# Kernel tuning notes

Hardware: AMD Instinct MI355X
Metric: run time of the kernel (lower is better)

## Reference

```python
import jax, jax.numpy as jnp
import numpy as np

N_NODES = 50000
IN_FEAT = 64
HIDDEN = 128
OUT = 10
N_EDGES = 800000


def setup_inputs() -> dict:
    key = jax.random.key(0)
    ks = jax.random.split(key, 8)
    s = lambda fan_in: 1.0 / np.sqrt(fan_in)
    x = jax.random.normal(ks[0], (N_NODES, IN_FEAT), dtype=jnp.float32)
    edge_index = jax.random.randint(ks[1], (2, N_EDGES), 0, N_NODES, dtype=jnp.int32)
    # SAGEConv params: lin_l (neighbor path, has bias) and lin_r (root path, no bias)
    W1l = jax.random.uniform(ks[2], (HIDDEN, IN_FEAT), jnp.float32, -s(IN_FEAT), s(IN_FEAT))
    b1 = jnp.zeros((HIDDEN,), jnp.float32)
    W1r = jax.random.uniform(ks[3], (HIDDEN, IN_FEAT), jnp.float32, -s(IN_FEAT), s(IN_FEAT))
    W2l = jax.random.uniform(ks[4], (OUT, HIDDEN), jnp.float32, -s(HIDDEN), s(HIDDEN))
    b2 = jnp.zeros((OUT,), jnp.float32)
    W2r = jax.random.uniform(ks[5], (OUT, HIDDEN), jnp.float32, -s(HIDDEN), s(HIDDEN))
    return {"x": x, "edge_index": edge_index, "W1l": W1l, "b1": b1, "W1r": W1r,
            "W2l": W2l, "b2": b2, "W2r": W2r}


def _sage_conv(x, src, dst, Wl, b, Wr, num_nodes):
    # mean-aggregate neighbor features (src -> dst), then linear + root linear
    msgs = x[src]                                                    # [E, d]
    agg = jax.ops.segment_sum(msgs, dst, num_segments=num_nodes)     # [N, d]
    cnt = jax.ops.segment_sum(jnp.ones((src.shape[0],), x.dtype), dst,
                              num_segments=num_nodes)                 # [N]
    mean = agg / jnp.maximum(cnt, 1.0)[:, None]
    return mean @ Wl.T + b + x @ Wr.T


def reference(x, edge_index, W1l, b1, W1r, W2l, b2, W2r):
    src, dst = edge_index[0], edge_index[1]
    n = x.shape[0]
    h = jax.nn.relu(_sage_conv(x, src, dst, W1l, b1, W1r, n))   # [N, hidden]
    h = _sage_conv(h, src, dst, W2l, b2, W2r, n)                 # [N, 10]
    # sum over nodes (transpose(0,1) then sum dim=1 == sum over axis 0)
    return jnp.sum(h, axis=0).reshape(1, OUT)
```

## Files before the change

### kernel.cpp

```cpp
#include <hip/hip_runtime.h>
#include <hip/hip_fp8.h>


constexpr int N = 50000;
constexpr int F = 64;
constexpr int H = 128;
constexpr int O = 10;
constexpr int E = 800000;

constexpr int NBUK = 391;
constexpr int CAPC = 2528;
constexpr int ADEPTH = 16;
constexpr int GSTR = 4;
constexpr int SPLIT = 4;

constexpr int NTILE = (N + 63) / 64;
constexpr int NB_TRANS = 391;

constexpr int GBIN_LEN  = NBUK * CAPC;
constexpr int GCUR_LEN  = NBUK * GSTR;
constexpr int MEANH_LEN = N * F / 2;
constexpr int XQ_LEN    = N * F / 4;
constexpr size_t WS_NEED_Q =
    (size_t)GBIN_LEN * 2 + GCUR_LEN * 2 + 2 * H + N + N + MEANH_LEN + XQ_LEN;

typedef _Float16 half2v __attribute__((ext_vector_type(2)));

__device__ __forceinline__ unsigned short f32_to_bf16_rne(float f) {
  unsigned u = __float_as_uint(f);
  u += 0x7FFFu + ((u >> 16) & 1u);
  return (unsigned short)(u >> 16);
}

__device__ __forceinline__ unsigned pack2h(float a, float b) {
  half2v h;
  h.x = (_Float16)a;
  h.y = (_Float16)b;
  return __builtin_bit_cast(unsigned, h);
}

__device__ __forceinline__ float dot2h(unsigned a, unsigned b, float c) {
#if __has_builtin(__builtin_amdgcn_fdot2)
  return __builtin_amdgcn_fdot2(__builtin_bit_cast(half2v, a),
                                __builtin_bit_cast(half2v, b), c, false);
#else
  const half2v ha = __builtin_bit_cast(half2v, a);
  const half2v hb = __builtin_bit_cast(half2v, b);
  c = fmaf((float)ha.x, (float)hb.x, c);
  return fmaf((float)ha.y, (float)hb.y, c);
#endif
}

__global__ __launch_bounds__(256) void k_cast(
    const float* __restrict__ x, unsigned* __restrict__ xq4) {
  const int tid = blockIdx.x * blockDim.x + threadIdx.x;
  const int stride = gridDim.x * blockDim.x;
  for (int i = tid; i < N * F / 4; i += stride) {
    const float4 v = reinterpret_cast<const float4*>(x)[i];
    const __hip_fp8_e4m3 a(v.x), b(v.y), c(v.z), d(v.w);
    const unsigned o = (unsigned)a.__x | ((unsigned)b.__x << 8) |
                       ((unsigned)c.__x << 16) | ((unsigned)d.__x << 24);
    __builtin_nontemporal_store(o, xq4 + i);
  }
}

__global__ __launch_bounds__(256) void k_coarse(
    const int* __restrict__ ei, int* __restrict__ gcur,
    unsigned* __restrict__ gbin, int* __restrict__ gcur2,
    unsigned* __restrict__ gbin2) {
  __shared__ int scnt[NBUK];
  __shared__ unsigned stage[NBUK * ADEPTH];
  __shared__ int scnt2[NBUK];
  __shared__ unsigned stage2[NBUK * ADEPTH];
  const int tid = threadIdx.x;
  const int lane = tid & 63;
  const int wv = tid >> 6;
  for (int i = tid; i < NBUK; i += 256) { scnt[i] = 0; scnt2[i] = 0; }
  __syncthreads();

  const int chunk = E / 256;
  const int base = blockIdx.x * chunk;
  const int end = base + chunk;
  for (int e = base + tid; e < end; e += 256) {
    const int s = ei[e];
    const int d = ei[E + e];
    {
      const int b = d >> 7;
      const unsigned p = ((unsigned)s << 7) | (unsigned)(d & 127);
      const int pos = atomicAdd(&scnt[b], 1);
      if (pos < ADEPTH) {
        stage[b * ADEPTH + pos] = p;
      } else {
        const int g = atomicAdd(&gcur[b * GSTR], 1);
        if (g < CAPC) gbin[(size_t)b * CAPC + g] = p;
      }
    }
    {
      const int b2 = s >> 7;
      const unsigned p2 = ((unsigned)d << 7) | (unsigned)(s & 127);
      const int pos2 = atomicAdd(&scnt2[b2], 1);
      if (pos2 < ADEPTH) {
        stage2[b2 * ADEPTH + pos2] = p2;
      } else {
        const int g2 = atomicAdd(&gcur2[b2 * GSTR], 1);
        if (g2 < CAPC) gbin2[(size_t)b2 * CAPC + g2] = p2;
      }
    }
  }
  __syncthreads();

  for (int b0 = wv * 64 + lane; b0 < NBUK; b0 += 256) {
    int cnt = scnt[b0];
    if (cnt > ADEPTH) cnt = ADEPTH;
    if (cnt > 0) {
      const int gbase = atomicAdd(&gcur[b0 * GSTR], cnt);
      for (int k = 0; k < cnt; ++k) {
        const int g = gbase + k;
        if (g < CAPC) gbin[(size_t)b0 * CAPC + g] = stage[b0 * ADEPTH + k];
      }
    }
    int cnt2 = scnt2[b0];
    if (cnt2 > ADEPTH) cnt2 = ADEPTH;
    if (cnt2 > 0) {
      const int gbase2 = atomicAdd(&gcur2[b0 * GSTR], cnt2);
      for (int k = 0; k < cnt2; ++k) {
        const int g2 = gbase2 + k;
        if (g2 < CAPC) gbin2[(size_t)b0 * CAPC + g2] = stage2[b0 * ADEPTH + k];
      }
    }
  }
}

template <bool USE_Q>
__global__ __launch_bounds__(512) void k_agg2(
    const float* __restrict__ x, const unsigned char* __restrict__ xq,
    const int* __restrict__ gcur, const unsigned* __restrict__ gbin,
    unsigned short* __restrict__ mean1h, float* __restrict__ winv_g) {
  __shared__ int fcnt[32];
  __shared__ float winv_s[32];
  __shared__ unsigned short fbin[32][64];
  const int tid = threadIdx.x;
  const int lane = tid & 63;
  const int wv = __builtin_amdgcn_readfirstlane((int)(tid >> 6));
  const int b = blockIdx.x >> 2;
  const int part = blockIdx.x & 3;
  int mb = gcur[b * GSTR];
  if (mb > CAPC) mb = CAPC;

  if (tid < 32) fcnt[tid] = 0;
  __syncthreads();

  const unsigned* __restrict__ gb = gbin + (size_t)b * CAPC;
#define READF(I)                                                      \
  {                                                                   \
    unsigned P = 0;                                                   \
    const bool v = tid + (I) * 512 < mb;                              \
    if (v) P = gb[tid + (I) * 512];                                   \
    const int row = (int)(P & 127u);                                  \
    if (v && ((row >> 5) == part)) {                                  \
      const int dl = row & 31;                                        \
      const int pos = atomicAdd(&fcnt[dl], 1);                        \
      if (pos < 46) fbin[dl][pos] = (unsigned short)(P >> 7);         \
    }                                                                 \
  }
  READF(0) READF(1) READF(2) READF(3) READF(4)
#undef READF
  __syncthreads();

  if (tid < 32) {
    const int c = fcnt[tid];
    const float wv_ = 1.0f / (float)(c > 0 ? c : 1);
    winv_s[tid] = wv_;
    const int n = b * 128 + part * 32 + tid;
    if (n < N) winv_g[n] = wv_;
  }
  __syncthreads();

  #pragma unroll
  for (int r = 0; r < 4; ++r) {
    const int row = wv * 4 + r;
    const int n = b * 128 + part * 32 + row;
    if (n >= N) break;
    int m = __builtin_amdgcn_readfirstlane(fcnt[row]);
    const float winv = winv_s[row];
    if (m > 46) m = 46;
    const uint4* __restrict__ lq = reinterpret_cast<const uint4*>(&fbin[row][0]);
    const uint4 q0 = lq[0], q1 = lq[1], q2 = lq[2];
    const uint4 q3 = lq[3], q4 = lq[4], q5 = lq[5];
    float acc = 0.f;
#define DO2(U, base)                                                      \
    {                                                                     \
      const unsigned u = __builtin_amdgcn_readfirstlane(U);               \
      int sa = (int)(u & 0xFFFFu), sb = (int)(u >> 16);                   \
      sa = sa < N ? sa : 0;  sb = sb < N ? sb : 0;     \
      float va, vb;                                                       \
      if constexpr (USE_Q) {                                              \
        va = (float)*reinterpret_cast<const __hip_fp8_e4m3*>(             \
                 &xq[(size_t)sa * F + lane]);                             \
        vb = (float)*reinterpret_cast<const __hip_fp8_e4m3*>(             \
                 &xq[(size_t)sb * F + lane]);                             \
      } else {                                                            \
        va = x[(size_t)sa * F + lane];                                    \
        vb = x[(size_t)sb * F + lane];                                    \
      }                                                                   \
      acc += ((base) < m) ? va : 0.f;                                     \
      acc += ((base) + 1 < m) ? vb : 0.f;                                 \
    }
    if (m > 0)  { DO2(q0.x, 0)  DO2(q0.y, 2)  DO2(q0.z, 4)  DO2(q0.w, 6)  }
    if (m > 8)  { DO2(q1.x, 8)  DO2(q1.y, 10) DO2(q1.z, 12) DO2(q1.w, 14) }
    if (m > 16) { DO2(q2.x, 16) DO2(q2.y, 18) DO2(q2.z, 20) DO2(q2.w, 22) }
    if (m > 24) { DO2(q3.x, 24) DO2(q3.y, 26) DO2(q3.z, 28) DO2(q3.w, 30) }
    if (m > 32) { DO2(q4.x, 32) DO2(q4.y, 34) DO2(q4.z, 36) DO2(q4.w, 38) }
    if (m > 40) { DO2(q5.x, 40) DO2(q5.y, 42) DO2(q5.z, 44) }
#undef DO2
    mean1h[(size_t)n * F + lane] = f32_to_bf16_rne(acc * winv);
  }
}

__global__ __launch_bounds__(512) void k_wsum(
    const int* __restrict__ gcur2, const unsigned* __restrict__ gbin2,
    const float* __restrict__ winv_g, float* __restrict__ wsum) {
  __shared__ float lsum[128];
  const int tid = threadIdx.x;
  const int b = blockIdx.x;
  int mb = gcur2[b * GSTR];
  if (mb > CAPC) mb = CAPC;
  if (tid < 128) lsum[tid] = 0.f;
  __syncthreads();
  const unsigned* __restrict__ gb = gbin2 + (size_t)b * CAPC;
  #pragma unroll
  for (int i = 0; i < 5; ++i) {
    const int idx = tid + i * 512;
    if (idx < mb) {
      const unsigned p = gb[idx];
      atomicAdd(&lsum[p & 127u], winv_g[p >> 7]);
    }
  }
  __syncthreads();
  const int n = b * 128 + tid;
  if (tid < 128 && n < N) wsum[n] = lsum[tid];
}

__global__ __launch_bounds__(256) void k_trans(
    const float* __restrict__ x, const unsigned short* __restrict__ mean1h,
    const float* __restrict__ wsum,
    const float* __restrict__ W1l, const float* __restrict__ b1,
    const float* __restrict__ W1r,
    float* __restrict__ S_h, float* __restrict__ S_hw) {
  __shared__ unsigned smem[12288];
  unsigned short* feat_h = reinterpret_cast<unsigned short*>(smem);
  unsigned* wBh = smem + 4096;
  const int tid = threadIdx.x;
  const int tm = tid >> 4;
  const int tj = tid & 15;

  #pragma unroll
  for (int u = 0; u < 8; ++u) {
    const int idx = u * 256 + tid;
    const int jj = idx >> 4;
    const int k4 = idx & 15;
    const float4 vl = *reinterpret_cast<const float4*>(&W1l[jj * F + k4 * 4]);
    const float4 vr = *reinterpret_cast<const float4*>(&W1r[jj * F + k4 * 4]);
    wBh[(k4 * 2 + 0) * 128 + jj] = pack2h(vl.x, vl.y);
    wBh[(k4 * 2 + 1) * 128 + jj] = pack2h(vl.z, vl.w);
    wBh[(32 + k4 * 2 + 0) * 128 + jj] = pack2h(vr.x, vr.y);
    wBh[(32 + k4 * 2 + 1) * 128 + jj] = pack2h(vr.z, vr.w);
  }
  const float4 b1v0 = *reinterpret_cast<const float4*>(&b1[tj * 4]);
  const float4 b1v1 = *reinterpret_cast<const float4*>(&b1[64 + tj * 4]);

  float accS[8] = {0.f, 0.f, 0.f, 0.f, 0.f, 0.f, 0.f, 0.f};
  float accW[8] = {0.f, 0.f, 0.f, 0.f, 0.f, 0.f, 0.f, 0.f};

  for (int t = blockIdx.x; t < NTILE; t += NB_TRANS) {
    const int nbase = t * 64;
    __syncthreads();

    #pragma unroll
    for (int u = 0; u < 8; ++u) {
      const int idx = u * 256 + tid;
      const int nn = idx >> 5;
      const int q = idx & 31;
      const int gn = nbase + nn;
      ushort4 o;
      o.x = 0; o.y = 0; o.z = 0; o.w = 0;
      if (gn < N) {
        float f0, f1, f2, f3;
        if (q < 16) {
          const ushort4 t4 = reinterpret_cast<const ushort4*>(mean1h + (size_t)gn * F)[q];
          f0 = __uint_as_float((unsigned)t4.x << 16);
          f1 = __uint_as_float((unsigned)t4.y << 16);
          f2 = __uint_as_float((unsigned)t4.z << 16);
          f3 = __uint_as_float((unsigned)t4.w << 16);
        } else {
          const float4 v = reinterpret_cast<const float4*>(x + (size_t)gn * F)[q - 16];
          f0 = v.x; f1 = v.y; f2 = v.z; f3 = v.w;
        }
        const unsigned p01 = pack2h(f0, f1);
        const unsigned p23 = pack2h(f2, f3);
        o.x = (unsigned short)(p01 & 0xFFFFu);
        o.y = (unsigned short)(p01 >> 16);
        o.z = (unsigned short)(p23 & 0xFFFFu);
        o.w = (unsigned short)(p23 >> 16);
      }
      const int qs = q ^ ((nn >> 2) & 15);
      *reinterpret_cast<ushort4*>(&feat_h[nn * 128 + qs * 4]) = o;
    }
    __syncthreads();

    float acc[4][8] = {{0.f}};
    #pragma unroll 4
    for (int k4 = 0; k4 < 32; ++k4) {
      uint2 a[4];
      #pragma unroll
      for (int r = 0; r < 4; ++r) {
        const int ks = k4 ^ tm;
        a[r] = *reinterpret_cast<const uint2*>(&feat_h[(tm * 4 + r) * 128 + ks * 4]);
      }
      const uint4 B00 = *reinterpret_cast<const uint4*>(&wBh[(k4 * 2 + 0) * 128 + tj * 4]);
      const uint4 B10 = *reinterpret_cast<const uint4*>(&wBh[(k4 * 2 + 1) * 128 + tj * 4]);
      const uint4 B01 = *reinterpret_cast<const uint4*>(&wBh[(k4 * 2 + 0) * 128 + 64 + tj * 4]);
      const uint4 B11 = *reinterpret_cast<const uint4*>(&wBh[(k4 * 2 + 1) * 128 + 64 + tj * 4]);
      #pragma unroll
      for (int r = 0; r < 4; ++r) {
        acc[r][0] = dot2h(a[r].x, B00.x, acc[r][0]);
        acc[r][0] = dot2h(a[r].y, B10.x, acc[r][0]);
        acc[r][1] = dot2h(a[r].x, B00.y, acc[r][1]);
        acc[r][1] = dot2h(a[r].y, B10.y, acc[r][1]);
        acc[r][2] = dot2h(a[r].x, B00.z, acc[r][2]);
        acc[r][2] = dot2h(a[r].y, B10.z, acc[r][2]);
        acc[r][3] = dot2h(a[r].x, B00.w, acc[r][3]);
        acc[r][3] = dot2h(a[r].y, B10.w, acc[r][3]);
        acc[r][4] = dot2h(a[r].x, B01.x, acc[r][4]);
        acc[r][4] = dot2h(a[r].y, B11.x, acc[r][4]);
        acc[r][5] = dot2h(a[r].x, B01.y, acc[r][5]);
        acc[r][5] = dot2h(a[r].y, B11.y, acc[r][5]);
        acc[r][6] = dot2h(a[r].x, B01.z, acc[r][6]);
        acc[r][6] = dot2h(a[r].y, B11.z, acc[r][6]);
        acc[r][7] = dot2h(a[r].x, B01.w, acc[r][7]);
        acc[r][7] = dot2h(a[r].y, B11.w, acc[r][7]);
      }
    }

    #pragma unroll
    for (int r = 0; r < 4; ++r) {
      const int gn = nbase + tm * 4 + r;
      const bool valid = (gn < N);
      const float wsn = valid ? wsum[gn] : 0.f;
      const float bb[8] = {b1v0.x, b1v0.y, b1v0.z, b1v0.w,
                           b1v1.x, b1v1.y, b1v1.z, b1v1.w};
      #pragma unroll
      for (int c = 0; c < 8; ++c) {
        const float h = valid ? fmaxf(acc[r][c] + bb[c], 0.f) : 0.f;
        accS[c] += h;
        accW[c] = fmaf(wsn, h, accW[c]);
      }
    }
  }

  __syncthreads();
  float* redS = reinterpret_cast<float*>(smem);
  float* redW = reinterpret_cast<float*>(smem) + 2048;
  #pragma unroll
  for (int c = 0; c < 8; ++c) {
    const int j = (c < 4) ? (tj * 4 + c) : (64 + tj * 4 + (c - 4));
    redS[tm * 128 + j] = accS[c];
    redW[tm * 128 + j] = accW[c];
  }
  __syncthreads();
  if (tid < 128) {
    float s = 0.f, w = 0.f;
    #pragma unroll
    for (int m = 0; m < 16; ++m) {
      s += redS[m * 128 + tid];
      w += redW[m * 128 + tid];
    }
    atomicAdd(&S_h[tid], s);
    atomicAdd(&S_hw[tid], w);
  }
}

__global__ __launch_bounds__(64) void k_final(
    const float* __restrict__ S_h, const float* __restrict__ S_hw,
    const float* __restrict__ W2l, const float* __restrict__ b2,
    const float* __restrict__ W2r, float* __restrict__ out) {
  const int j = threadIdx.x;
  if (j < O) {
    float acc = (float)N * b2[j];
    #pragma unroll 8
    for (int k = 0; k < H; ++k)
      acc += S_hw[k] * W2l[j * H + k] + S_h[k] * W2r[j * H + k];
    out[j] = acc;
  }
}

extern "C" void kernel_launch(void* const* d_in, const int* in_sizes, int n_in,
                              void* d_out, int out_size, void* d_ws, size_t ws_size,
                              hipStream_t stream) {
  const float* x   = (const float*)d_in[0];
  const int*   ei  = (const int*)d_in[1];
  const float* W1l = (const float*)d_in[2];
  const float* b1  = (const float*)d_in[3];
  const float* W1r = (const float*)d_in[4];
  const float* W2l = (const float*)d_in[5];
  const float* b2  = (const float*)d_in[6];
  const float* W2r = (const float*)d_in[7];
  float* out = (float*)d_out;
  float* ws  = (float*)d_ws;

  const bool use_q = ws_size >= WS_NEED_Q * 4;

  size_t off = 0;
  unsigned* gbin = (unsigned*)ws; off += GBIN_LEN;
  unsigned* gbin2 = (unsigned*)(ws + off); off += GBIN_LEN;
  int* gcur = (int*)(ws + off); off += GCUR_LEN;
  int* gcur2 = (int*)(ws + off); off += GCUR_LEN;
  float* S_h = ws + off; off += H;
  float* S_hw = ws + off; off += H;
  float* winv_g = ws + off; off += N;
  float* wsum = ws + off; off += N;
  unsigned short* mean1h = (unsigned short*)(ws + off); off += MEANH_LEN;
  unsigned char* xq = nullptr;
  if (use_q) { xq = (unsigned char*)(ws + off); off += XQ_LEN; }

  (void)hipMemsetAsync(gcur, 0, (size_t)(GCUR_LEN * 2 + 2 * H) * 4, stream);
  if (use_q)
    hipLaunchKernelGGL(k_cast, dim3(512), dim3(256), 0, stream,
                       x, (unsigned*)xq);
  hipLaunchKernelGGL(k_coarse, dim3(256), dim3(256), 0, stream,
                     ei, gcur, gbin, gcur2, gbin2);
  if (use_q) {
    hipLaunchKernelGGL(k_agg2<true>, dim3(NBUK * SPLIT), dim3(512), 0, stream,
                       x, xq, gcur, gbin, mean1h, winv_g);
  } else {
    hipLaunchKernelGGL(k_agg2<false>, dim3(NBUK * SPLIT), dim3(512), 0, stream,
                       x, xq, gcur, gbin, mean1h, winv_g);
  }
  hipLaunchKernelGGL(k_wsum, dim3(NBUK), dim3(512), 0, stream,
                     gcur2, gbin2, winv_g, wsum);
  hipLaunchKernelGGL(k_trans, dim3(NB_TRANS), dim3(256), 0, stream,
                     x, mean1h, wsum, W1l, b1, W1r, S_h, S_hw);
  hipLaunchKernelGGL(k_final, dim3(1), dim3(64), 0, stream,
                     S_h, S_hw, W2l, b2, W2r, out);
}
```

Measured before the change: 117.1 us.

## Split transform kernel by output half per tile and fold memset into cast kernel

The transform kernel drops its persistent loop over 64-node tiles. It now launches one block per tile and per half of the 128 hidden outputs, so each block stages only half the weights and keeps a 4x4 accumulator. This gives more parallelism, smaller LDS use and fewer registers, but each half reloads the same feature tile and issues more atomics. The separate hipMemsetAsync is removed and the zeroing is done at the start of the cast kernel, saving one operation in the launch sequence.

```diff
diff --git a/kernel.cpp b/kernel.cpp
--- a/kernel.cpp
+++ b/kernel.cpp
@@ -15,10 +15,11 @@
 constexpr int SPLIT = 4;
 
 constexpr int NTILE = (N + 63) / 64;
-constexpr int NB_TRANS = 391;
+constexpr int NB_TRANS = NTILE * 2;
 
 constexpr int GBIN_LEN  = NBUK * CAPC;
 constexpr int GCUR_LEN  = NBUK * GSTR;
+constexpr int ZLEN      = GCUR_LEN * 2 + 2 * H;
 constexpr int MEANH_LEN = N * F / 2;
 constexpr int XQ_LEN    = N * F / 4;
 constexpr size_t WS_NEED_Q =
@@ -52,8 +53,11 @@
 }
 
 __global__ __launch_bounds__(256) void k_cast(
-    const float* __restrict__ x, unsigned* __restrict__ xq4) {
+    const float* __restrict__ x, unsigned* __restrict__ xq4,
+    float* __restrict__ zbase, int do_cast) {
   const int tid = blockIdx.x * blockDim.x + threadIdx.x;
+  if (tid < ZLEN) zbase[tid] = 0.0f;
+  if (!do_cast) return;
   const int stride = gridDim.x * blockDim.x;
   for (int i = tid; i < N * F / 4; i += stride) {
     const float4 v = reinterpret_cast<const float4*>(x)[i];
@@ -247,136 +251,121 @@
     const float* __restrict__ W1l, const float* __restrict__ b1,
     const float* __restrict__ W1r,
     float* __restrict__ S_h, float* __restrict__ S_hw) {
-  __shared__ unsigned smem[12288];
+  __shared__ unsigned smem[8192];
   unsigned short* feat_h = reinterpret_cast<unsigned short*>(smem);
   unsigned* wBh = smem + 4096;
   const int tid = threadIdx.x;
+  const int t = blockIdx.x >> 1;
+  const int jhalf = blockIdx.x & 1;
+  const int jbase = jhalf * 64;
   const int tm = tid >> 4;
   const int tj = tid & 15;
-
-  #pragma unroll
-  for (int u = 0; u < 8; ++u) {
+  const int nbase = t * 64;
+
+  #pragma unroll
+  for (int u = 0; u < 4; ++u) {
     const int idx = u * 256 + tid;
     const int jj = idx >> 4;
     const int k4 = idx & 15;
-    const float4 vl = *reinterpret_cast<const float4*>(&W1l[jj * F + k4 * 4]);
-    const float4 vr = *reinterpret_cast<const float4*>(&W1r[jj * F + k4 * 4]);
-    wBh[(k4 * 2 + 0) * 128 + jj] = pack2h(vl.x, vl.y);
-    wBh[(k4 * 2 + 1) * 128 + jj] = pack2h(vl.z, vl.w);
-    wBh[(32 + k4 * 2 + 0) * 128 + jj] = pack2h(vr.x, vr.y);
-    wBh[(32 + k4 * 2 + 1) * 128 + jj] = pack2h(vr.z, vr.w);
-  }
-  const float4 b1v0 = *reinterpret_cast<const float4*>(&b1[tj * 4]);
-  const float4 b1v1 = *reinterpret_cast<const float4*>(&b1[64 + tj * 4]);
-
-  float accS[8] = {0.f, 0.f, 0.f, 0.f, 0.f, 0.f, 0.f, 0.f};
-  float accW[8] = {0.f, 0.f, 0.f, 0.f, 0.f, 0.f, 0.f, 0.f};
-
-  for (int t = blockIdx.x; t < NTILE; t += NB_TRANS) {
-    const int nbase = t * 64;
-    __syncthreads();
-
-    #pragma unroll
-    for (int u = 0; u < 8; ++u) {
-      const int idx = u * 256 + tid;
-      const int nn = idx >> 5;
-      const int q = idx & 31;
-      const int gn = nbase + nn;
-      ushort4 o;
-      o.x = 0; o.y = 0; o.z = 0; o.w = 0;
-      if (gn < N) {
-        float f0, f1, f2, f3;
-        if (q < 16) {
-          const ushort4 t4 = reinterpret_cast<const ushort4*>(mean1h + (size_t)gn * F)[q];
-          f0 = __uint_as_float((unsigned)t4.x << 16);
-          f1 = __uint_as_float((unsigned)t4.y << 16);
-          f2 = __uint_as_float((unsigned)t4.z << 16);
-          f3 = __uint_as_float((unsigned)t4.w << 16);
-        } else {
-          const float4 v = reinterpret_cast<const float4*>(x + (size_t)gn * F)[q - 16];
-          f0 = v.x; f1 = v.y; f2 = v.z; f3 = v.w;
-        }
-        const unsigned p01 = pack2h(f0, f1);
-        const unsigned p23 = pack2h(f2, f3);
-        o.x = (unsigned short)(p01 & 0xFFFFu);
-        o.y = (unsigned short)(p01 >> 16);
-        o.z = (unsigned short)(p23 & 0xFFFFu);
-        o.w = (unsigned short)(p23 >> 16);
+    const float4 vl = *reinterpret_cast<const float4*>(&W1l[(jbase + jj) * F + k4 * 4]);
+    const float4 vr = *reinterpret_cast<const float4*>(&W1r[(jbase + jj) * F + k4 * 4]);
+    wBh[(k4 * 2 + 0) * 64 + jj] = pack2h(vl.x, vl.y);
+    wBh[(k4 * 2 + 1) * 64 + jj] = pack2h(vl.z, vl.w);
+    wBh[(32 + k4 * 2 + 0) * 64 + jj] = pack2h(vr.x, vr.y);
+    wBh[(32 + k4 * 2 + 1) * 64 + jj] = pack2h(vr.z, vr.w);
+  }
+
+  #pragma unroll
+  for (int u = 0; u < 8; ++u) {
+    const int idx = u * 256 + tid;
+    const int nn = idx >> 5;
+    const int q = idx & 31;
+    const int gn = nbase + nn;
+    ushort4 o;
+    o.x = 0; o.y = 0; o.z = 0; o.w = 0;
+    if (gn < N) {
+      float f0, f1, f2, f3;
+      if (q < 16) {
+        const ushort4 t4 = reinterpret_cast<const ushort4*>(mean1h + (size_t)gn * F)[q];
+        f0 = __uint_as_float((unsigned)t4.x << 16);
+        f1 = __uint_as_float((unsigned)t4.y << 16);
+        f2 = __uint_as_float((unsigned)t4.z << 16);
+        f3 = __uint_as_float((unsigned)t4.w << 16);
+      } else {
+        const float4 v = reinterpret_cast<const float4*>(x + (size_t)gn * F)[q - 16];
+        f0 = v.x; f1 = v.y; f2 = v.z; f3 = v.w;
       }
-      const int qs = q ^ ((nn >> 2) & 15);
-      *reinterpret_cast<ushort4*>(&feat_h[nn * 128 + qs * 4]) = o;
-    }
-    __syncthreads();
-
-    float acc[4][8] = {{0.f}};
-    #pragma unroll 4
-    for (int k4 = 0; k4 < 32; ++k4) {
-      uint2 a[4];
-      #pragma unroll
-      for (int r = 0; r < 4; ++r) {
-        const int ks = k4 ^ tm;
-        a[r] = *reinterpret_cast<const uint2*>(&feat_h[(tm * 4 + r) * 128 + ks * 4]);
-      }
-      const uint4 B00 = *reinterpret_cast<const uint4*>(&wBh[(k4 * 2 + 0) * 128 + tj * 4]);
-      const uint4 B10 = *reinterpret_cast<const uint4*>(&wBh[(k4 * 2 + 1) * 128 + tj * 4]);
-      const uint4 B01 = *reinterpret_cast<const uint4*>(&wBh[(k4 * 2 + 0) * 128 + 64 + tj * 4]);
-      const uint4 B11 = *reinterpret_cast<const uint4*>(&wBh[(k4 * 2 + 1) * 128 + 64 + tj * 4]);
-      #pragma unroll
-      for (int r = 0; r < 4; ++r) {
-        acc[r][0] = dot2h(a[r].x, B00.x, acc[r][0]);
-        acc[r][0] = dot2h(a[r].y, B10.x, acc[r][0]);
-        acc[r][1] = dot2h(a[r].x, B00.y, acc[r][1]);
-        acc[r][1] = dot2h(a[r].y, B10.y, acc[r][1]);
-        acc[r][2] = dot2h(a[r].x, B00.z, acc[r][2]);
-        acc[r][2] = dot2h(a[r].y, B10.z, acc[r][2]);
-        acc[r][3] = dot2h(a[r].x, B00.w, acc[r][3]);
-        acc[r][3] = dot2h(a[r].y, B10.w, acc[r][3]);
-        acc[r][4] = dot2h(a[r].x, B01.x, acc[r][4]);
-        acc[r][4] = dot2h(a[r].y, B11.x, acc[r][4]);
-        acc[r][5] = dot2h(a[r].x, B01.y, acc[r][5]);
-        acc[r][5] = dot2h(a[r].y, B11.y, acc[r][5]);
-        acc[r][6] = dot2h(a[r].x, B01.z, acc[r][6]);
-        acc[r][6] = dot2h(a[r].y, B11.z, acc[r][6]);
-        acc[r][7] = dot2h(a[r].x, B01.w, acc[r][7]);
-        acc[r][7] = dot2h(a[r].y, B11.w, acc[r][7]);
-      }
-    }
-
+      const unsigned p01 = pack2h(f0, f1);
+      const unsigned p23 = pack2h(f2, f3);
+      o.x = (unsigned short)(p01 & 0xFFFFu);
+      o.y = (unsigned short)(p01 >> 16);
+      o.z = (unsigned short)(p23 & 0xFFFFu);
+      o.w = (unsigned short)(p23 >> 16);
+    }
+    const int qs = q ^ ((nn >> 2) & 15);
+    *reinterpret_cast<ushort4*>(&feat_h[nn * 128 + qs * 4]) = o;
+  }
+  __syncthreads();
+
+  float acc[4][4] = {{0.f}};
+  #pragma unroll 4
+  for (int k4 = 0; k4 < 32; ++k4) {
+    uint2 a[4];
     #pragma unroll
     for (int r = 0; r < 4; ++r) {
-      const int gn = nbase + tm * 4 + r;
-      const bool valid = (gn < N);
-      const float wsn = valid ? wsum[gn] : 0.f;
-      const float bb[8] = {b1v0.x, b1v0.y, b1v0.z, b1v0.w,
-                           b1v1.x, b1v1.y, b1v1.z, b1v1.w};
-      #pragma unroll
-      for (int c = 0; c < 8; ++c) {
-        const float h = valid ? fmaxf(acc[r][c] + bb[c], 0.f) : 0.f;
-        accS[c] += h;
-        accW[c] = fmaf(wsn, h, accW[c]);
-      }
+      const int ks = k4 ^ tm;
+      a[r] = *reinterpret_cast<const uint2*>(&feat_h[(tm * 4 + r) * 128 + ks * 4]);
+    }
+    const uint4 B0 = *reinterpret_cast<const uint4*>(&wBh[(k4 * 2 + 0) * 64 + tj * 4]);
+    const uint4 B1 = *reinterpret_cast<const uint4*>(&wBh[(k4 * 2 + 1) * 64 + tj * 4]);
+    #pragma unroll
+    for (int r = 0; r < 4; ++r) {
+      acc[r][0] = dot2h(a[r].x, B0.x, acc[r][0]);
+      acc[r][0] = dot2h(a[r].y, B1.x, acc[r][0]);
+      acc[r][1] = dot2h(a[r].x, B0.y, acc[r][1]);
+      acc[r][1] = dot2h(a[r].y, B1.y, acc[r][1]);
+      acc[r][2] = dot2h(a[r].x, B0.z, acc[r][2]);
+      acc[r][2] = dot2h(a[r].y, B1.z, acc[r][2]);
+      acc[r][3] = dot2h(a[r].x, B0.w, acc[r][3]);
+      acc[r][3] = dot2h(a[r].y, B1.w, acc[r][3]);
+    }
+  }
+
+  const float4 b1v = *reinterpret_cast<const float4*>(&b1[jbase + tj * 4]);
+  float accS[4] = {0.f, 0.f, 0.f, 0.f};
+  float accW[4] = {0.f, 0.f, 0.f, 0.f};
+  const float bb[4] = {b1v.x, b1v.y, b1v.z, b1v.w};
+  #pragma unroll
+  for (int r = 0; r < 4; ++r) {
+    const int gn = nbase + tm * 4 + r;
+    const bool valid = (gn < N);
+    const float wsn = valid ? wsum[gn] : 0.f;
+    #pragma unroll
+    for (int c = 0; c < 4; ++c) {
+      const float h = valid ? fmaxf(acc[r][c] + bb[c], 0.f) : 0.f;
+      accS[c] += h;
+      accW[c] = fmaf(wsn, h, accW[c]);
     }
   }
 
   __syncthreads();
   float* redS = reinterpret_cast<float*>(smem);
-  float* redW = reinterpret_cast<float*>(smem) + 2048;
-  #pragma unroll
-  for (int c = 0; c < 8; ++c) {
-    const int j = (c < 4) ? (tj * 4 + c) : (64 + tj * 4 + (c - 4));
-    redS[tm * 128 + j] = accS[c];
-    redW[tm * 128 + j] = accW[c];
-  }
-  __syncthreads();
-  if (tid < 128) {
+  float* redW = reinterpret_cast<float*>(smem) + 1024;
+  #pragma unroll
+  for (int c = 0; c < 4; ++c) {
+    redS[tm * 64 + tj * 4 + c] = accS[c];
+    redW[tm * 64 + tj * 4 + c] = accW[c];
+  }
+  __syncthreads();
+  if (tid < 64) {
     float s = 0.f, w = 0.f;
     #pragma unroll
     for (int m = 0; m < 16; ++m) {
-      s += redS[m * 128 + tid];
-      w += redW[m * 128 + tid];
-    }
-    atomicAdd(&S_h[tid], s);
-    atomicAdd(&S_hw[tid], w);
+      s += redS[m * 64 + tid];
+      w += redW[m * 64 + tid];
+    }
+    atomicAdd(&S_h[jbase + tid], s);
+    atomicAdd(&S_hw[jbase + tid], w);
   }
 }
 
@@ -423,10 +412,8 @@
   unsigned char* xq = nullptr;
   if (use_q) { xq = (unsigned char*)(ws + off); off += XQ_LEN; }
 
-  (void)hipMemsetAsync(gcur, 0, (size_t)(GCUR_LEN * 2 + 2 * H) * 4, stream);
-  if (use_q)
-    hipLaunchKernelGGL(k_cast, dim3(512), dim3(256), 0, stream,
-                       x, (unsigned*)xq);
+  hipLaunchKernelGGL(k_cast, dim3(512), dim3(256), 0, stream,
+                     x, (unsigned*)xq, (float*)gcur, use_q ? 1 : 0);
   hipLaunchKernelGGL(k_coarse, dim3(256), dim3(256), 0, stream,
                      ei, gcur, gbin, gcur2, gbin2);
   if (use_q) {
```

Result: no change. 115.5 us (-1.4%).
